# Optimization experiments

Measured on AMD Instinct MI355X. Metric: run time of the kernel, lower is better.

## Reference

```python
import jax, jax.numpy as jnp
import numpy as np

B, Q, K = 4, 128, 1024
DQ, DK, DV, H = 512, 512, 512, 256
NEG_INF = -1e6


def setup_inputs() -> dict:
    key = jax.random.key(0)
    ks = jax.random.split(key, 6)
    queries = jax.random.normal(ks[0], (B, Q, DQ), dtype=jnp.float32)
    keys = jax.random.normal(ks[1], (B, K, DK), dtype=jnp.float32)
    values = jax.random.normal(ks[2], (B, K, DV), dtype=jnp.float32)
    valid_lens = jax.random.randint(ks[3], (B,), 1, K + 1, dtype=jnp.int32)
    # Learned params (Dense use_bias=False): W_q [DQ,H], W_k [DK,H], w_v [H] (Dense(1) squeezed)
    Wq = jax.random.normal(ks[4], (DQ, H), dtype=jnp.float32) / np.sqrt(DQ)
    Wk = jax.random.normal(ks[5], (DK, H), dtype=jnp.float32) / np.sqrt(DK)
    wv = jax.random.normal(jax.random.fold_in(key, 7), (H,), dtype=jnp.float32) / np.sqrt(H)
    return {"queries": queries, "keys": keys, "values": values,
            "valid_lens": valid_lens, "Wq": Wq, "Wk": Wk, "wv": wv}


def reference(queries, keys, values, valid_lens, Wq, Wk, wv):
    q = queries @ Wq                       # [B,Q,H]
    k = keys @ Wk                          # [B,K,H]
    feats = jnp.tanh(q[:, :, None, :] + k[:, None, :, :])   # [B,Q,K,H]
    scores = jnp.einsum('bqkh,h->bqk', feats, wv)            # [B,Q,K]
    mask = jnp.arange(scores.shape[-1]) < valid_lens[:, None, None]  # [B,1,K]
    scores = jnp.where(mask, scores, NEG_INF)
    attn = jax.nn.softmax(scores, axis=-1)                   # [B,Q,K]
    # dropout is identity at inference
    return attn @ values                                     # [B,Q,DV]
```

## Files before the change

kernel.cpp:

```cpp
#include <hip/hip_runtime.h>

#define Bn 4
#define Qn 128
#define Kn 1024
#define Dn 512
#define Hn 256
#define SCALE 2.8853900817779268f
#define LOG2E 1.4426950408889634f

typedef __attribute__((ext_vector_type(8))) short short8;
typedef __attribute__((ext_vector_type(4))) float floatx4;

__device__ __forceinline__ unsigned short f2bf(float x) {
    unsigned int u = __float_as_uint(x);
    return (unsigned short)((u + 0x7fffu + ((u >> 16) & 1u)) >> 16);
}

__global__ __launch_bounds__(256) void prep_kernel(
    const float* __restrict__ queries, const float* __restrict__ keys,
    const float* __restrict__ Wq, const float* __restrict__ Wk,
    unsigned short* __restrict__ qk16,
    unsigned short* __restrict__ wtq, unsigned short* __restrict__ wtk)
{
    const int blk = blockIdx.x;
    const int t = threadIdx.x;
    if (blk < 64) {
        __shared__ float s_t[64][68];
        const int wsel = blk >> 5;
        const int tile = blk & 31;
        const int r0 = (tile >> 2) * 64;
        const int c0 = (tile & 3) * 64;
        const float* W = wsel ? Wk : Wq;
        unsigned short* Wt = wsel ? wtk : wtq;
        #pragma unroll
        for (int i = 0; i < 4; ++i) {
            int idx = t + i * 256;
            int row = idx >> 4, c4 = idx & 15;
            float4 v = *(const float4*)(W + (size_t)(r0 + row) * Hn + c0 + c4 * 4);
            s_t[row][c4*4+0] = v.x; s_t[row][c4*4+1] = v.y;
            s_t[row][c4*4+2] = v.z; s_t[row][c4*4+3] = v.w;
        }
        __syncthreads();
        const int n = c0 + (t >> 2);
        const int seg = t & 3;
        unsigned short tmp[16];
        #pragma unroll
        for (int i = 0; i < 16; ++i)
            tmp[i] = f2bf(s_t[seg * 16 + i][t >> 2]);
        uint4* dst = (uint4*)(Wt + (size_t)n * Dn + r0 + seg * 16);
        dst[0] = ((uint4*)tmp)[0];
        dst[1] = ((uint4*)tmp)[1];
    } else {
        const int cblk = blk - 64;
        const float* src = (cblk < 64) ? (queries + (size_t)cblk * 4096)
                                       : (keys + (size_t)(cblk - 64) * 4096);
        const float* s = src + t * 16;
        unsigned short tmp[16];
        #pragma unroll
        for (int i = 0; i < 4; ++i) {
            float4 v = *(const float4*)(s + i * 4);
            tmp[i*4+0] = f2bf(v.x); tmp[i*4+1] = f2bf(v.y);
            tmp[i*4+2] = f2bf(v.z); tmp[i*4+3] = f2bf(v.w);
        }
        uint4* dst = (uint4*)(qk16 + (size_t)cblk * 4096 + t * 16);
        dst[0] = ((uint4*)tmp)[0];
        dst[1] = ((uint4*)tmp)[1];
    }
}

__global__ __launch_bounds__(256) void proj_mfma_kernel(
    const unsigned short* __restrict__ qk16,
    const unsigned short* __restrict__ wtq,
    const unsigned short* __restrict__ wtk,
    const int* __restrict__ valid_lens,
    float* __restrict__ qproj, float* __restrict__ kprojT)
{
    const int blk = blockIdx.x;
    const int nt = blk & 3;
    const int mt = blk >> 2;
    const int n0 = nt * 64;
    int arow0, drow0; const unsigned short* Wt; bool is_q;
    if (mt < 8) {
        arow0 = mt * 64; drow0 = arow0; Wt = wtq; is_q = true;
    } else {
        int r0 = (mt - 8) * 64;
        if ((r0 & 1023) >= valid_lens[r0 >> 10]) return;
        arow0 = 512 + r0; drow0 = r0; Wt = wtk; is_q = false;
    }
    const int t = threadIdx.x;
    const int lane = t & 63;
    const int w = t >> 6;

    __shared__ float s_x[64 * 68];
    short8* s_a = (short8*)s_x;
    short8* s_b = (short8*)(s_x + 2048);

    int arow[2], brow[2], acol[2];
    #pragma unroll
    for (int i = 0; i < 2; ++i) {
        int s = t + i * 256;
        int grp = s >> 6, l = s & 63;
        int top = grp >> 1, kc = grp & 1;
        arow[i] = arow0 + top * 16 + (l & 15);
        brow[i] = n0 + top * 16 + (l & 15);
        acol[i] = kc * 32 + ((l >> 4) << 3);
    }

    floatx4 z = {0.f, 0.f, 0.f, 0.f};
    floatx4 acc0 = z, acc1 = z, acc2 = z, acc3 = z;

    for (int kt = 0; kt < 8; ++kt) {
        __syncthreads();
        #pragma unroll
        for (int i = 0; i < 2; ++i) {
            s_a[t + i*256] = *(const short8*)(qk16 + (size_t)arow[i] * Dn + kt*64 + acol[i]);
            s_b[t + i*256] = *(const short8*)(Wt   + (size_t)brow[i] * Dn + kt*64 + acol[i]);
        }
        __syncthreads();
        #pragma unroll
        for (int kc = 0; kc < 2; ++kc) {
            short8 a  = s_a[(w*2 + kc)*64 + lane];
            short8 b0 = s_b[(0  + kc)*64 + lane];
            short8 b1 = s_b[(2  + kc)*64 + lane];
            short8 b2 = s_b[(4  + kc)*64 + lane];
            short8 b3 = s_b[(6  + kc)*64 + lane];
            acc0 = __builtin_amdgcn_mfma_f32_16x16x32_bf16(a, b0, acc0, 0, 0, 0);
            acc1 = __builtin_amdgcn_mfma_f32_16x16x32_bf16(a, b1, acc1, 0, 0, 0);
            acc2 = __builtin_amdgcn_mfma_f32_16x16x32_bf16(a, b2, acc2, 0, 0, 0);
            acc3 = __builtin_amdgcn_mfma_f32_16x16x32_bf16(a, b3, acc3, 0, 0, 0);
        }
    }

    floatx4 av[4] = {acc0, acc1, acc2, acc3};
    if (is_q) {
        const int mrow = drow0 + w * 16 + ((lane >> 4) << 2);
        const int ncol = n0 + (lane & 15);
        float* dp = qproj + (size_t)mrow * Hn + ncol;
        #pragma unroll
        for (int g = 0; g < 4; ++g)
            #pragma unroll
            for (int r = 0; r < 4; ++r)
                dp[(size_t)r * Hn + g * 16] = av[g][r] * SCALE;
    } else {
        __syncthreads();
        #pragma unroll
        for (int g = 0; g < 4; ++g) {
            const int n_loc = g * 16 + (lane & 15);
            const int m_base = w * 16 + ((lane >> 4) << 2);
            #pragma unroll
            for (int r = 0; r < 4; ++r)
                s_x[n_loc * 68 + m_base + r] = av[g][r] * SCALE;
        }
        __syncthreads();
        const int bq = drow0 >> 10;
        const int kk0 = drow0 & 1023;
        float* dstT = kprojT + ((size_t)bq * Hn + n0) * Kn + kk0;
        #pragma unroll
        for (int i = 0; i < 4; ++i) {
            int f4 = t + i * 256;
            int row = f4 >> 4, c4 = f4 & 15;
            *(float4*)(dstT + (size_t)row * Kn + c4 * 4) =
                *(const float4*)&s_x[row * 68 + c4 * 4];
        }
    }
}

__global__ __launch_bounds__(256) void score_kernel(
    const float* __restrict__ qproj, const float* __restrict__ kprojT,
    const float* __restrict__ wv, const int* __restrict__ valid_lens,
    float* __restrict__ escores, float* __restrict__ rowsum)
{
    const int blk = blockIdx.x;
    const int kt = blk & 15;
    const int qt = (blk >> 4) & 31;
    const int b  = blk >> 9;
    const int vlen = valid_lens[b];
    const int k0 = kt * 64;
    if (k0 >= vlen) return;
    const int t = threadIdx.x;
    const int wave = __builtin_amdgcn_readfirstlane(t >> 6);
    const int lane = t & 63;
    const int qrow = qt * 4 + wave;

    const float* qb = qproj + (size_t)(b * Qn + qrow) * Hn;
    const float* kb = kprojT + (size_t)b * Hn * Kn + k0 + lane;

    float sumw = wv[lane] + wv[lane + 64] + wv[lane + 128] + wv[lane + 192];
    #pragma unroll
    for (int off = 32; off; off >>= 1)
        sumw += __shfl_xor(sumw, off, 64);

    float acc = 0.f;
    #pragma unroll 8
    for (int h = 0; h < Hn; ++h) {
        float kv = kb[(size_t)h * Kn];
        float qv = qb[h];
        float wvh = wv[h];
        acc = fmaf(wvh, __builtin_amdgcn_rcpf(1.f + exp2f(qv + kv)), acc);
    }
    float s = sumw - 2.f * acc;

    const int k = k0 + lane;
    float e = (k < vlen) ? exp2f(s * LOG2E) : 0.f;
    if (k < vlen)
        escores[(size_t)(b * Qn + qrow) * Kn + k] = e;
    #pragma unroll
    for (int off = 32; off; off >>= 1)
        e += __shfl_xor(e, off, 64);
    if (lane == 0)
        atomicAdd(&rowsum[b * Qn + qrow], e);
}

__global__ __launch_bounds__(256) void av_kernel(
    const float* __restrict__ escores, const float* __restrict__ values,
    float* __restrict__ parts)
{
    const int blk = blockIdx.x;
    const int kc = blk & 3;
    const int dh = (blk >> 2) & 1;
    const int qt = (blk >> 3) & 15;
    const int b  = blk >> 7;
    const int t = threadIdx.x;
    const int q0 = qt * 8, kb = kc * 256, d = dh * 256 + t;

    const int ebase = __builtin_amdgcn_readfirstlane((b * Qn + q0) * Kn + kb);
    const float* vb = values + ((size_t)b * Kn + kb) * Dn + d;

    float acc[8] = {0.f, 0.f, 0.f, 0.f, 0.f, 0.f, 0.f, 0.f};
    #pragma unroll 2
    for (int k = 0; k < 256; k += 4) {
        float v0 = vb[(size_t)(k + 0) * Dn];
        float v1 = vb[(size_t)(k + 1) * Dn];
        float v2 = vb[(size_t)(k + 2) * Dn];
        float v3 = vb[(size_t)(k + 3) * Dn];
        #pragma unroll
        for (int j = 0; j < 8; ++j) {
            float4 e4 = *(const float4*)(escores + ebase + j * Kn + k);
            acc[j] += e4.x * v0 + e4.y * v1 + e4.z * v2 + e4.w * v3;
        }
    }
    float* pp = parts + (size_t)kc * (Bn * Qn * Dn) + (size_t)(b * Qn + q0) * Dn + d;
    #pragma unroll
    for (int j = 0; j < 8; ++j)
        pp[(size_t)j * Dn] = acc[j];
}

__global__ __launch_bounds__(256) void reduce_kernel(
    const float* __restrict__ parts, const float* __restrict__ rowsum,
    float* __restrict__ out)
{
    const int idx = blockIdx.x * 256 + threadIdx.x;
    const int row = (idx * 4) >> 9;
    const float inv = __builtin_amdgcn_rcpf(rowsum[row]);
    const float4* p = (const float4*)parts;
    float4 a = p[idx];
    float4 b = p[idx + 65536];
    float4 c = p[idx + 131072];
    float4 d = p[idx + 196608];
    float4 o;
    o.x = (a.x + b.x + c.x + d.x) * inv;
    o.y = (a.y + b.y + c.y + d.y) * inv;
    o.z = (a.z + b.z + c.z + d.z) * inv;
    o.w = (a.w + b.w + c.w + d.w) * inv;
    ((float4*)out)[idx] = o;
}

extern "C" void kernel_launch(void* const* d_in, const int* in_sizes, int n_in,
                              void* d_out, int out_size, void* d_ws, size_t ws_size,
                              hipStream_t stream) {
    const float* queries    = (const float*)d_in[0];
    const float* keys       = (const float*)d_in[1];
    const float* values     = (const float*)d_in[2];
    const int*   valid_lens = (const int*)  d_in[3];
    const float* Wq         = (const float*)d_in[4];
    const float* Wk         = (const float*)d_in[5];
    const float* wv         = (const float*)d_in[6];
    float* out = (float*)d_out;

    float* qproj   = (float*)d_ws;
    float* kprojT  = qproj + Bn * Qn * Hn;
    float* escores = kprojT + Bn * Hn * Kn;
    float* rowsum  = escores + Bn * Qn * Kn;
    float* parts   = rowsum + Bn * Qn;
    unsigned short* qk16 = (unsigned short*)(parts + 4 * Bn * Qn * Dn);
    unsigned short* wtq  = qk16 + 4608 * 512;
    unsigned short* wtk  = wtq + 256 * 512;

    hipMemsetAsync(escores, 0, (size_t)(Bn * Qn * Kn + Bn * Qn) * sizeof(float),
                   stream);
    prep_kernel<<<640, 256, 0, stream>>>(queries, keys, Wq, Wk, qk16, wtq, wtk);
    proj_mfma_kernel<<<288, 256, 0, stream>>>(qk16, wtq, wtk, valid_lens,
                                              qproj, kprojT);
    score_kernel<<<2048, 256, 0, stream>>>(qproj, kprojT, wv, valid_lens,
                                           escores, rowsum);
    av_kernel<<<512, 256, 0, stream>>>(escores, values, parts);
    reduce_kernel<<<256, 256, 0, stream>>>(parts, rowsum, out);
}
```

Baseline: 174.4 us.

## Compute four query rows per wave in score kernel with prefetched key loads

Each wave now handles four query rows instead of one, so every key-projection value it loads is reused four times. The grid shrinks from 2048 to 512 blocks. Key values for the next block of 8 hidden dims are loaded one step ahead to hide memory latency. The kernel is dominated by exp and rcp work, so less load traffic may matter little, and the smaller grid of 512 blocks of 256 threads gives fewer waves to spread across the device's compute units.

```diff
diff --git a/kernel.cpp b/kernel.cpp
--- a/kernel.cpp
+++ b/kernel.cpp
@@ -172,17 +172,17 @@
 {
     const int blk = blockIdx.x;
     const int kt = blk & 15;
-    const int qt = (blk >> 4) & 31;
-    const int b  = blk >> 9;
+    const int qt = (blk >> 4) & 7;
+    const int b  = blk >> 7;
     const int vlen = valid_lens[b];
     const int k0 = kt * 64;
     if (k0 >= vlen) return;
     const int t = threadIdx.x;
     const int wave = __builtin_amdgcn_readfirstlane(t >> 6);
     const int lane = t & 63;
-    const int qrow = qt * 4 + wave;
-
-    const float* qb = qproj + (size_t)(b * Qn + qrow) * Hn;
+    const int qrow0 = qt * 16 + wave * 4;
+
+    const float* qb = qproj + (size_t)(b * Qn + qrow0) * Hn;
     const float* kb = kprojT + (size_t)b * Hn * Kn + k0 + lane;
 
     float sumw = wv[lane] + wv[lane + 64] + wv[lane + 128] + wv[lane + 192];
@@ -190,25 +190,52 @@
     for (int off = 32; off; off >>= 1)
         sumw += __shfl_xor(sumw, off, 64);
 
-    float acc = 0.f;
-    #pragma unroll 8
-    for (int h = 0; h < Hn; ++h) {
-        float kv = kb[(size_t)h * Kn];
-        float qv = qb[h];
-        float wvh = wv[h];
-        acc = fmaf(wvh, __builtin_amdgcn_rcpf(1.f + exp2f(qv + kv)), acc);
-    }
-    float s = sumw - 2.f * acc;
+    float acc[4] = {0.f, 0.f, 0.f, 0.f};
+    float kv[8];
+    #pragma unroll
+    for (int i = 0; i < 8; ++i)
+        kv[i] = kb[(size_t)i * Kn];
+
+    #pragma unroll 1
+    for (int hb = 0; hb < Hn; hb += 8) {
+        float cur[8];
+        #pragma unroll
+        for (int i = 0; i < 8; ++i) cur[i] = kv[i];
+        if (hb + 8 < Hn) {
+            #pragma unroll
+            for (int i = 0; i < 8; ++i)
+                kv[i] = kb[(size_t)(hb + 8 + i) * Kn];
+        }
+        asm volatile("" ::: "memory");
+        #pragma unroll
+        for (int i = 0; i < 8; ++i) {
+            const int h = hb + i;
+            const float wvh = wv[h];
+            const float q0 = qb[0 * Hn + h];
+            const float q1 = qb[1 * Hn + h];
+            const float q2 = qb[2 * Hn + h];
+            const float q3 = qb[3 * Hn + h];
+            acc[0] = fmaf(wvh, __builtin_amdgcn_rcpf(1.f + exp2f(q0 + cur[i])), acc[0]);
+            acc[1] = fmaf(wvh, __builtin_amdgcn_rcpf(1.f + exp2f(q1 + cur[i])), acc[1]);
+            acc[2] = fmaf(wvh, __builtin_amdgcn_rcpf(1.f + exp2f(q2 + cur[i])), acc[2]);
+            acc[3] = fmaf(wvh, __builtin_amdgcn_rcpf(1.f + exp2f(q3 + cur[i])), acc[3]);
+        }
+    }
 
     const int k = k0 + lane;
-    float e = (k < vlen) ? exp2f(s * LOG2E) : 0.f;
-    if (k < vlen)
-        escores[(size_t)(b * Qn + qrow) * Kn + k] = e;
-    #pragma unroll
-    for (int off = 32; off; off >>= 1)
-        e += __shfl_xor(e, off, 64);
-    if (lane == 0)
-        atomicAdd(&rowsum[b * Qn + qrow], e);
+    const bool ok = (k < vlen);
+    float* ep = escores + (size_t)(b * Qn + qrow0) * Kn + k;
+    #pragma unroll
+    for (int r = 0; r < 4; ++r) {
+        float s = sumw - 2.f * acc[r];
+        float e = ok ? exp2f(s * LOG2E) : 0.f;
+        if (ok) ep[(size_t)r * Kn] = e;
+        #pragma unroll
+        for (int off = 32; off; off >>= 1)
+            e += __shfl_xor(e, off, 64);
+        if (lane == 0)
+            atomicAdd(&rowsum[b * Qn + qrow0 + r], e);
+    }
 }
 
 __global__ __launch_bounds__(256) void av_kernel(
@@ -291,8 +318,8 @@
     prep_kernel<<<640, 256, 0, stream>>>(queries, keys, Wq, Wk, qk16, wtq, wtk);
     proj_mfma_kernel<<<288, 256, 0, stream>>>(qk16, wtq, wtk, valid_lens,
                                               qproj, kprojT);
-    score_kernel<<<2048, 256, 0, stream>>>(qproj, kprojT, wv, valid_lens,
-                                           escores, rowsum);
+    score_kernel<<<512, 256, 0, stream>>>(qproj, kprojT, wv, valid_lens,
+                                          escores, rowsum);
     av_kernel<<<512, 256, 0, stream>>>(escores, values, parts);
     reduce_kernel<<<256, 256, 0, stream>>>(parts, rowsum, out);
 }
```

Result: no change. 173.3 us (-0.6%).
